# Performance work log

Measured on AMD Instinct MI355X. Metric: run time of the kernel, lower is better.

Reference implementation:

```python
import jax, jax.numpy as jnp
import numpy as np


def _overlap_add_fft_conv(signal, kernel):
    """Vectorized overlap-add FFT convolution.

    signal: (B, K, T) float; kernel: (B, K, R) float.
    Returns (B, K, T), identical math to the torch per-block loop (the
    ortho-normed rfft/irfft pair on the signal cancels, kernel rfft uses
    default backward norm, exactly as in the original code).
    """
    B, K, T = signal.shape
    R = kernel.shape[-1]
    fft_len = 2 << (R - 1).bit_length()          # e.g. R=4000 -> 8192
    step = fft_len - R + 1                        # hop between blocks
    pad_len = (-T) % step                         # pad T up to multiple of step
    L = T + pad_len
    n_blocks = L // step

    # split padded signal into non-overlapping blocks, zero-pad each to fft_len
    sig = jnp.pad(signal, ((0, 0), (0, 0), (0, pad_len)))
    blocks = sig.reshape(B, K, n_blocks, step)
    blocks = jnp.pad(blocks, ((0, 0), (0, 0), (0, 0), (0, fft_len - step)))

    kernel_fft = jnp.fft.rfft(
        jnp.pad(kernel, ((0, 0), (0, 0), (0, fft_len - R))))      # (B,K,F)
    block_fft = jnp.fft.rfft(blocks, norm='ortho')                # (B,K,n_blocks,F)
    conv = jnp.fft.irfft(block_fft * kernel_fft[:, :, None, :],
                         norm='ortho')                            # (B,K,n_blocks,fft_len)

    # overlap-add: block i contributes at offset i*step, length fft_len
    idx = jnp.arange(n_blocks)[:, None] * step + jnp.arange(fft_len)[None, :]
    out = jnp.zeros((B, K, L + R - 1), dtype=conv.dtype)
    out = out.at[:, :, idx].add(conv)
    return out[:, :, :T]


def setup_inputs() -> dict:
    key = jax.random.key(0)
    k1, k2 = jax.random.split(key)
    onsets = jax.random.normal(k1, (8, 8, 262144), dtype=jnp.float32)
    sources = jax.random.normal(k2, (8, 8, 4000), dtype=jnp.float32)
    return {"onsets": onsets, "sources": sources, "delay_compensation": 0}


def reference(onsets, sources, delay_compensation):
    # delay_compensation is unused in the original module as well
    return _overlap_add_fft_conv(onsets, sources)
```

## Files before the change

kernel.cpp:

```cpp
#include <hip/hip_runtime.h>

#define T_LEN 262144
#define R_LEN 4000
#define NCH 64
#define NCHUNK 253
#define WIN_SLOTS 4608
#define LDS_BYTES 73984

typedef __attribute__((ext_vector_type(8))) short bf16x8;
typedef __attribute__((ext_vector_type(16))) float f32x16;

static __device__ __forceinline__ unsigned short f2bf(float f) {
  unsigned u = __builtin_bit_cast(unsigned, f);
  unsigned r = 0x7FFFu + ((u >> 16) & 1u);
  return (unsigned short)((u + r) >> 16);
}

__global__ __launch_bounds__(256) void build_btf(const float* __restrict__ src,
                                                 unsigned short* __restrict__ btf) {
  int t0 = blockIdx.x * 256 + threadIdx.x;
  if (t0 >= NCH * NCHUNK * 64) return;
  int lane = t0 & 63;
  int t = (t0 >> 6) % NCHUNK;
  int ch = t0 / (64 * NCHUNK);
  int j = lane & 31;
  int h = lane >> 5;
  int kbase = 4000 + j - 16 * t - 8 * h;
  const float* k = src + (size_t)ch * R_LEN;
  unsigned short vals[8];
#pragma unroll
  for (int e = 0; e < 8; ++e) {
    int r = kbase - e;
    float f = (r >= 0 && r < R_LEN) ? k[r] : 0.0f;
    vals[e] = f2bf(f);
  }
  unsigned int* dst = (unsigned int*)(btf + (size_t)t0 * 8);
  dst[0] = (unsigned int)vals[0] | ((unsigned int)vals[1] << 16);
  dst[1] = (unsigned int)vals[2] | ((unsigned int)vals[3] << 16);
  dst[2] = (unsigned int)vals[4] | ((unsigned int)vals[5] << 16);
  dst[3] = (unsigned int)vals[6] | ((unsigned int)vals[7] << 16);
}

__global__ __launch_bounds__(256, 2) void conv_main(const float* __restrict__ x,
                                                    const unsigned short* __restrict__ btf,
                                                    float* __restrict__ out) {
  __shared__ alignas(16) unsigned char xs[LDS_BYTES];
  const int bid = blockIdx.x;
  const int ch = bid & 63;
  const int T0 = (bid >> 6) << 15;
  const float* xch = x + (size_t)ch * T_LEN;

  for (int s = threadIdx.x; s < WIN_SLOTS; s += 256) {
    int gi = T0 - 4000 + 8 * s;
    float v0, v1, v2, v3, v4, v5, v6, v7;
    if (gi >= 0 && gi + 8 <= T_LEN) {
      float4 a = *(const float4*)(xch + gi);
      float4 b = *(const float4*)(xch + gi + 4);
      v0 = a.x; v1 = a.y; v2 = a.z; v3 = a.w;
      v4 = b.x; v5 = b.y; v6 = b.z; v7 = b.w;
    } else {
      v0 = (gi + 0 >= 0 && gi + 0 < T_LEN) ? xch[gi + 0] : 0.f;
      v1 = (gi + 1 >= 0 && gi + 1 < T_LEN) ? xch[gi + 1] : 0.f;
      v2 = (gi + 2 >= 0 && gi + 2 < T_LEN) ? xch[gi + 2] : 0.f;
      v3 = (gi + 3 >= 0 && gi + 3 < T_LEN) ? xch[gi + 3] : 0.f;
      v4 = (gi + 4 >= 0 && gi + 4 < T_LEN) ? xch[gi + 4] : 0.f;
      v5 = (gi + 5 >= 0 && gi + 5 < T_LEN) ? xch[gi + 5] : 0.f;
      v6 = (gi + 6 >= 0 && gi + 6 < T_LEN) ? xch[gi + 6] : 0.f;
      v7 = (gi + 7 >= 0 && gi + 7 < T_LEN) ? xch[gi + 7] : 0.f;
    }
    uint4 pk;
    pk.x = (unsigned int)f2bf(v0) | ((unsigned int)f2bf(v1) << 16);
    pk.y = (unsigned int)f2bf(v2) | ((unsigned int)f2bf(v3) << 16);
    pk.z = (unsigned int)f2bf(v4) | ((unsigned int)f2bf(v5) << 16);
    pk.w = (unsigned int)f2bf(v6) | ((unsigned int)f2bf(v7) << 16);
    int beta = s >> 1;
    int bp = (((beta >> 3) + (beta & 7) * 289) << 5) + 16 * (s & 1);
    *(uint4*)(xs + bp) = pk;
  }
  __syncthreads();

  const int lane = threadIdx.x & 63;
  const int w = threadIdx.x >> 6;
  const int i = lane & 31;
  const int h = lane >> 5;
  const int lanepart = 32 * i + 16 * h;
  const char* bbase = (const char*)btf + ((size_t)ch * NCHUNK) * 1024 + (size_t)lane * 16;

  auto aread = [&](int m, int q) -> bf16x8 {
    int b0 = 512 * w + 256 * m + q;
    int addr = (((b0 >> 3) + (b0 & 7) * 289) << 5) + lanepart;
    return *(const bf16x8*)(xs + addr);
  };
  auto bload = [&](int t) -> bf16x8 {
    int tc = t > 252 ? 252 : t;
    return *(const bf16x8*)(bbase + (size_t)tc * 1024);
  };

  f32x16 acc[2][4] = {};
  bf16x8 zero8 = {};
  bf16x8 E0 = bload(0), E1 = zero8, E2 = zero8, E3 = zero8;
  bf16x8 O0 = bload(1), O1 = zero8, O2 = zero8, O3 = zero8;
  bf16x8 a0 = aread(0, 0), a1 = aread(1, 0);

#define DO_STEP(B0, B1, B2, B3, QQ)                                                      \
  {                                                                                      \
    bf16x8 nb = bload((QQ) + 2);                                                         \
    bf16x8 a0n = aread(0, (QQ) + 1);                                                     \
    bf16x8 a1n = aread(1, (QQ) + 1);                                                     \
    acc[0][0] = __builtin_amdgcn_mfma_f32_32x32x16_bf16(a0, B0, acc[0][0], 0, 0, 0);     \
    acc[0][1] = __builtin_amdgcn_mfma_f32_32x32x16_bf16(a0, B1, acc[0][1], 0, 0, 0);     \
    acc[0][2] = __builtin_amdgcn_mfma_f32_32x32x16_bf16(a0, B2, acc[0][2], 0, 0, 0);     \
    acc[0][3] = __builtin_amdgcn_mfma_f32_32x32x16_bf16(a0, B3, acc[0][3], 0, 0, 0);     \
    acc[1][0] = __builtin_amdgcn_mfma_f32_32x32x16_bf16(a1, B0, acc[1][0], 0, 0, 0);     \
    acc[1][1] = __builtin_amdgcn_mfma_f32_32x32x16_bf16(a1, B1, acc[1][1], 0, 0, 0);     \
    acc[1][2] = __builtin_amdgcn_mfma_f32_32x32x16_bf16(a1, B2, acc[1][2], 0, 0, 0);     \
    acc[1][3] = __builtin_amdgcn_mfma_f32_32x32x16_bf16(a1, B3, acc[1][3], 0, 0, 0);     \
    B3 = B2; B2 = B1; B1 = B0; B0 = nb;                                                  \
    a0 = a0n; a1 = a1n;                                                                  \
  }

#pragma unroll 4
  for (int q = 0; q < 258; q += 2) {
    DO_STEP(E0, E1, E2, E3, q);
    DO_STEP(O0, O1, O2, O3, q + 1);
  }
#undef DO_STEP

  float* och = out + (size_t)ch * T_LEN + T0 + 8192 * w;
#pragma unroll
  for (int m = 0; m < 2; ++m) {
#pragma unroll
    for (int c = 0; c < 4; ++c) {
#pragma unroll
      for (int r = 0; r < 16; ++r) {
        int row = (r & 3) + 8 * (r >> 2) + 4 * h;
        och[4096 * m + 32 * c + 128 * row + i] = acc[m][c][r];
      }
    }
  }
}

extern "C" void kernel_launch(void* const* d_in, const int* in_sizes, int n_in,
                              void* d_out, int out_size, void* d_ws, size_t ws_size,
                              hipStream_t stream) {
  const float* onsets  = (const float*)d_in[0];
  const float* sources = (const float*)d_in[1];
  unsigned short* btf  = (unsigned short*)d_ws;
  float* out = (float*)d_out;

  int nthr = NCH * NCHUNK * 64;
  build_btf<<<(nthr + 255) / 256, 256, 0, stream>>>(sources, btf);
  conv_main<<<512, 256, 0, stream>>>(onsets, btf, out);
}
```

Measured before the change: 115.1 us.

## Split conv work across 8 waves per block and linearize LDS fill stores

Doubles threads per block from 256 to 512 so each wave owns one 4096-sample M tile instead of two. That halves per-wave accumulators and A reads, and raises the waves available to hide MFMA and load latency. The LDS fill now iterates over physical slots and inverts the swizzle, so stores are contiguous. The B-operand (kernel) global loads are repeated by twice as many waves, which adds cache traffic.

After: 122.3 us. 1.06x slower.

```diff
diff --git a/kernel.cpp b/kernel.cpp
--- a/kernel.cpp
+++ b/kernel.cpp
@@ -4,7 +4,7 @@
 #define R_LEN 4000
 #define NCH 64
 #define NCHUNK 253
-#define WIN_SLOTS 4608
+#define NSLOT 4624
 #define LDS_BYTES 73984
 
 typedef __attribute__((ext_vector_type(8))) short bf16x8;
@@ -41,7 +41,7 @@
   dst[3] = (unsigned int)vals[6] | ((unsigned int)vals[7] << 16);
 }
 
-__global__ __launch_bounds__(256, 2) void conv_main(const float* __restrict__ x,
+__global__ __launch_bounds__(512, 4) void conv_main(const float* __restrict__ x,
                                                     const unsigned short* __restrict__ btf,
                                                     float* __restrict__ out) {
   __shared__ alignas(16) unsigned char xs[LDS_BYTES];
@@ -50,7 +50,11 @@
   const int T0 = (bid >> 6) << 15;
   const float* xch = x + (size_t)ch * T_LEN;
 
-  for (int s = threadIdx.x; s < WIN_SLOTS; s += 256) {
+  for (int n = threadIdx.x; n < NSLOT; n += 512) {
+    int pb = n >> 1;
+    int r = pb / 289;
+    int q = pb - 289 * r;
+    int s = 2 * (8 * q + r) + (n & 1);
     int gi = T0 - 4000 + 8 * s;
     float v0, v1, v2, v3, v4, v5, v6, v7;
     if (gi >= 0 && gi + 8 <= T_LEN) {
@@ -73,9 +77,7 @@
     pk.y = (unsigned int)f2bf(v2) | ((unsigned int)f2bf(v3) << 16);
     pk.z = (unsigned int)f2bf(v4) | ((unsigned int)f2bf(v5) << 16);
     pk.w = (unsigned int)f2bf(v6) | ((unsigned int)f2bf(v7) << 16);
-    int beta = s >> 1;
-    int bp = (((beta >> 3) + (beta & 7) * 289) << 5) + 16 * (s & 1);
-    *(uint4*)(xs + bp) = pk;
+    *(uint4*)(xs + 16 * n) = pk;
   }
   __syncthreads();
 
@@ -86,8 +88,8 @@
   const int lanepart = 32 * i + 16 * h;
   const char* bbase = (const char*)btf + ((size_t)ch * NCHUNK) * 1024 + (size_t)lane * 16;
 
-  auto aread = [&](int m, int q) -> bf16x8 {
-    int b0 = 512 * w + 256 * m + q;
+  auto aread = [&](int q) -> bf16x8 {
+    int b0 = 256 * w + q;
     int addr = (((b0 >> 3) + (b0 & 7) * 289) << 5) + lanepart;
     return *(const bf16x8*)(xs + addr);
   };
@@ -96,27 +98,22 @@
     return *(const bf16x8*)(bbase + (size_t)tc * 1024);
   };
 
-  f32x16 acc[2][4] = {};
+  f32x16 acc[4] = {};
   bf16x8 zero8 = {};
   bf16x8 E0 = bload(0), E1 = zero8, E2 = zero8, E3 = zero8;
   bf16x8 O0 = bload(1), O1 = zero8, O2 = zero8, O3 = zero8;
-  bf16x8 a0 = aread(0, 0), a1 = aread(1, 0);
+  bf16x8 a = aread(0);
 
 #define DO_STEP(B0, B1, B2, B3, QQ)                                                      \
   {                                                                                      \
     bf16x8 nb = bload((QQ) + 2);                                                         \
-    bf16x8 a0n = aread(0, (QQ) + 1);                                                     \
-    bf16x8 a1n = aread(1, (QQ) + 1);                                                     \
-    acc[0][0] = __builtin_amdgcn_mfma_f32_32x32x16_bf16(a0, B0, acc[0][0], 0, 0, 0);     \
-    acc[0][1] = __builtin_amdgcn_mfma_f32_32x32x16_bf16(a0, B1, acc[0][1], 0, 0, 0);     \
-    acc[0][2] = __builtin_amdgcn_mfma_f32_32x32x16_bf16(a0, B2, acc[0][2], 0, 0, 0);     \
-    acc[0][3] = __builtin_amdgcn_mfma_f32_32x32x16_bf16(a0, B3, acc[0][3], 0, 0, 0);     \
-    acc[1][0] = __builtin_amdgcn_mfma_f32_32x32x16_bf16(a1, B0, acc[1][0], 0, 0, 0);     \
-    acc[1][1] = __builtin_amdgcn_mfma_f32_32x32x16_bf16(a1, B1, acc[1][1], 0, 0, 0);     \
-    acc[1][2] = __builtin_amdgcn_mfma_f32_32x32x16_bf16(a1, B2, acc[1][2], 0, 0, 0);     \
-    acc[1][3] = __builtin_amdgcn_mfma_f32_32x32x16_bf16(a1, B3, acc[1][3], 0, 0, 0);     \
+    bf16x8 an = aread((QQ) + 1);                                                         \
+    acc[0] = __builtin_amdgcn_mfma_f32_32x32x16_bf16(a, B0, acc[0], 0, 0, 0);            \
+    acc[1] = __builtin_amdgcn_mfma_f32_32x32x16_bf16(a, B1, acc[1], 0, 0, 0);            \
+    acc[2] = __builtin_amdgcn_mfma_f32_32x32x16_bf16(a, B2, acc[2], 0, 0, 0);            \
+    acc[3] = __builtin_amdgcn_mfma_f32_32x32x16_bf16(a, B3, acc[3], 0, 0, 0);            \
     B3 = B2; B2 = B1; B1 = B0; B0 = nb;                                                  \
-    a0 = a0n; a1 = a1n;                                                                  \
+    a = an;                                                                              \
   }
 
 #pragma unroll 4
@@ -126,16 +123,13 @@
   }
 #undef DO_STEP
 
-  float* och = out + (size_t)ch * T_LEN + T0 + 8192 * w;
+  float* och = out + (size_t)ch * T_LEN + T0 + 4096 * w;
 #pragma unroll
-  for (int m = 0; m < 2; ++m) {
+  for (int c = 0; c < 4; ++c) {
 #pragma unroll
-    for (int c = 0; c < 4; ++c) {
-#pragma unroll
-      for (int r = 0; r < 16; ++r) {
-        int row = (r & 3) + 8 * (r >> 2) + 4 * h;
-        och[4096 * m + 32 * c + 128 * row + i] = acc[m][c][r];
-      }
+    for (int r = 0; r < 16; ++r) {
+      int row = (r & 3) + 8 * (r >> 2) + 4 * h;
+      och[32 * c + 128 * row + i] = acc[c][r];
     }
   }
 }
@@ -150,5 +144,5 @@
 
   int nthr = NCH * NCHUNK * 64;
   build_btf<<<(nthr + 255) / 256, 256, 0, stream>>>(sources, btf);
-  conv_main<<<512, 256, 0, stream>>>(onsets, btf, out);
+  conv_main<<<512, 512, 0, stream>>>(onsets, btf, out);
 }
```
